# Optimization experiments

Hardware: AMD Instinct MI355X
Metric: run time of the kernel (lower is better)

The kernel has to match this reference:

```python
import jax, jax.numpy as jnp
import numpy as np
import math

B, P, N = 4, 8, 512
D_MODEL, H, D_K = 128, 4, 32
T_ALL = 4
WHICH_IDX = np.array([0, 1, 3])  # which_transition_matrices = [T,T,F,T]
T = 3
EPS = 1e-5


def setup_inputs() -> dict:
    key = jax.random.key(0)
    ks = jax.random.split(key, 12)
    inputs = jax.random.normal(ks[0], (B, P, N, D_MODEL), jnp.float32)
    c_inputs = jax.random.normal(ks[1], (B, P, N, D_MODEL), jnp.float32)
    vals = jax.random.uniform(ks[2], (T_ALL, N, N), jnp.float32)
    keep = (jax.random.uniform(ks[3], (T_ALL, N, N)) < 0.05).astype(jnp.float32)
    eye = jnp.eye(N, dtype=jnp.float32)
    transition_matrices = vals * keep * (1.0 - eye) + eye
    s = 1.0 / math.sqrt(D_MODEL)
    Wq = jax.random.normal(ks[4], (T, D_MODEL, D_MODEL), jnp.float32) * s
    Wk = jax.random.normal(ks[5], (T, D_MODEL, D_MODEL), jnp.float32) * s
    Wv = jax.random.normal(ks[6], (T, D_MODEL, D_MODEL), jnp.float32) * s
    Wo = jax.random.normal(ks[7], (D_MODEL, T * D_MODEL), jnp.float32) * (1.0 / math.sqrt(T * D_MODEL))
    ln_gamma = jnp.ones((D_MODEL,), jnp.float32)
    ln_beta = jnp.zeros((D_MODEL,), jnp.float32)
    return dict(inputs=inputs, c_inputs=c_inputs, transition_matrices=transition_matrices,
                Wq=Wq, Wk=Wk, Wv=Wv, Wo=Wo, ln_gamma=ln_gamma, ln_beta=ln_beta)


def reference(inputs, c_inputs, transition_matrices, Wq, Wk, Wv, Wo, ln_gamma, ln_beta):
    tm = transition_matrices[jnp.asarray(WHICH_IDX)]  # [T, N, N]
    # per-transition-matrix projections (torch Linear: x @ W.T), then split heads
    def proj(W):
        y = jnp.einsum('bpnd,tod->tbpno', inputs, W)
        return y.reshape(T, B, P, N, H, D_K)
    Q, K, V = proj(Wq), proj(Wk), proj(Wv)
    scores = jnp.einsum('tbpnhk,tbpmhk->tbphnm', Q, K) / math.sqrt(D_K)
    mask = jnp.where(tm != 0, 0.0, -jnp.inf)[:, None, None, None]  # [T,1,1,1,N,N]
    alpha = jax.nn.softmax(scores + mask, axis=-1)
    # post-softmax reweighting by transition matrix, then V matmul
    out = jnp.einsum('tbphnm,tbpmhk->tbpnhk', alpha * tm[:, None, None, None], V)
    out = out.reshape(T, B, P, N, D_MODEL)
    out = jnp.moveaxis(out, 0, -2).reshape(B, P, N, T * D_MODEL)  # concat over matrices
    out = jnp.einsum('bpnf,df->bpnd', out, Wo)  # final Linear (bias=False); dropout p=0
    res = out + inputs
    mu = res.mean(-1, keepdims=True)
    var = ((res - mu) ** 2).mean(-1, keepdims=True)
    return (res - mu) / jnp.sqrt(var + EPS) * ln_gamma + ln_beta
```

## Files before the change

### kernel.cpp

```cpp
#include <hip/hip_runtime.h>


typedef __attribute__((ext_vector_type(8))) short  short8;
typedef __attribute__((ext_vector_type(4))) float  floatx4;

#define WS_BIG   50331648ull
#define WS_XL    54919168ull
#define QSCALE   0.25503486f

__device__ __forceinline__ float b2f(unsigned short u) {
    union { unsigned int i; float f; } v; v.i = ((unsigned int)u) << 16; return v.f;
}
__device__ __forceinline__ unsigned short f2b(float f) {
    union { float f; unsigned int i; } v; v.f = f;
    unsigned int x = v.i;
    return (unsigned short)((x + 0x7fffu + ((x >> 16) & 1u)) >> 16);
}
__device__ __forceinline__ unsigned int fbits(float f) {
    union { float f; unsigned int i; } v; v.f = f; return v.i;
}
__device__ __forceinline__ short8 cvt8(const float* p) {
    floatx4 a = *(const floatx4*)p;
    floatx4 b = *(const floatx4*)(p + 4);
    short8 r;
    r[0] = (short)f2b(a[0]); r[1] = (short)f2b(a[1]);
    r[2] = (short)f2b(a[2]); r[3] = (short)f2b(a[3]);
    r[4] = (short)f2b(b[0]); r[5] = (short)f2b(b[1]);
    r[6] = (short)f2b(b[2]); r[7] = (short)f2b(b[3]);
    return r;
}

__global__ __launch_bounds__(256) void k_prep(
    const float* __restrict__ X,  const float* __restrict__ Wq,
    const float* __restrict__ Wk, const float* __restrict__ Wv,
    const float* __restrict__ Wo,
    unsigned short* __restrict__ Xb, unsigned short* __restrict__ Wb,
    unsigned short* __restrict__ Wob)
{
    size_t i = ((size_t)blockIdx.x * 256 + threadIdx.x) * 8;
    const float* src; unsigned short* dst; size_t off;
    if      (i < 2097152) { src = X;  dst = Xb;          off = i; }
    else if (i < 2146304) { src = Wq; dst = Wb;          off = i - 2097152; }
    else if (i < 2195456) { src = Wk; dst = Wb + 49152;  off = i - 2146304; }
    else if (i < 2244608) { src = Wv; dst = Wb + 98304;  off = i - 2195456; }
    else                  { src = Wo; dst = Wob;         off = i - 2244608; }
    *(short8*)&dst[off] = cvt8(&src[off]);
}

__global__ __launch_bounds__(256) void k_qkv_pre2(
    const unsigned short* __restrict__ Xb,
    const unsigned short* __restrict__ Wb,
    unsigned short* __restrict__ q_ws,
    unsigned short* __restrict__ k_ws,
    unsigned short* __restrict__ v_ws)
{
    int bp = blockIdx.x, mt = blockIdx.y, z = blockIdx.z;
    int qkv = z / 3, t = z % 3;
    __shared__ unsigned short Xs[128 * 128];
    __shared__ unsigned short Cs[4][32 * 128];
    int tid = threadIdx.x;
    int lane = tid & 63, wv = tid >> 6;
    int l15 = lane & 15, quad = lane >> 4;

    const unsigned short* Xbase = Xb + ((size_t)bp * 512 + mt * 128) * 128;
    for (int i = 0; i < 8; ++i) {
        int e = (i * 256 + tid) * 8;
        *(short8*)&Xs[e] = *(const short8*)&Xbase[e];
    }
    __syncthreads();

    unsigned short* Osel[3] = { q_ws, k_ws, v_ws };
    int rt0 = wv * 2, rt1 = wv * 2 + 1;

    const unsigned short* Wt = Wb + qkv * 49152 + t * 16384;
    unsigned short* Ob = Osel[qkv] + (size_t)t * 2097152
                       + ((size_t)bp * 512 + mt * 128 + wv * 32) * 128;
    float sc = (qkv == 0) ? QSCALE : 1.0f;

    for (int ct = 0; ct < 8; ++ct) {
        short8 bfr[4];
        for (int kk = 0; kk < 4; ++kk)
            bfr[kk] = *(const short8*)&Wt[(size_t)(ct * 16 + l15) * 128 + kk * 32 + quad * 8];
        floatx4 acc0 = {0.f, 0.f, 0.f, 0.f};
        floatx4 acc1 = {0.f, 0.f, 0.f, 0.f};
        for (int kk = 0; kk < 4; ++kk) {
            short8 a0 = *(const short8*)&Xs[(rt0 * 16 + l15) * 128 + kk * 32 + quad * 8];
            short8 a1 = *(const short8*)&Xs[(rt1 * 16 + l15) * 128 + kk * 32 + quad * 8];
            acc0 = __builtin_amdgcn_mfma_f32_16x16x32_bf16(a0, bfr[kk], acc0, 0, 0, 0);
            acc1 = __builtin_amdgcn_mfma_f32_16x16x32_bf16(a1, bfr[kk], acc1, 0, 0, 0);
        }
        #pragma unroll
        for (int i = 0; i < 4; ++i) {
            int row = quad * 4 + i;
            int swz = (row & 7) << 4;
            int col = (ct * 16 + l15) ^ swz;
            Cs[wv][row * 128 + col]        = f2b(acc0[i] * sc);
            Cs[wv][(16 + row) * 128 + col] = f2b(acc1[i] * sc);
        }
    }
    #pragma unroll
    for (int j = 0; j < 8; ++j) {
        int flat = j * 64 + lane;
        int r = flat >> 4;
        int cg = (flat & 15) * 8;
        int cgs = cg ^ ((r & 7) << 4);
        *(short8*)&Ob[(size_t)r * 128 + cg] = *(const short8*)&Cs[wv][r * 128 + cgs];
    }
}

__global__ __launch_bounds__(256) void k_qkv_cvt(
    const float* __restrict__ X,
    const float* __restrict__ Wq, const float* __restrict__ Wk,
    const float* __restrict__ Wv,
    unsigned short* __restrict__ q_ws, unsigned short* __restrict__ k_ws,
    unsigned short* __restrict__ v_ws,
    int wstride, int ostride)
{
    int bp = blockIdx.x, mt = blockIdx.y, tz = blockIdx.z;
    __shared__ unsigned short Xs[128 * 128];
    int tid = threadIdx.x;
    int lane = tid & 63, wv = tid >> 6;
    int l15 = lane & 15, quad = lane >> 4;

    const float* Xbase = X + ((size_t)bp * 512 + mt * 128) * 128;
    for (int i = 0; i < 8; ++i) {
        int e = (i * 256 + tid) * 8;
        *(short8*)&Xs[e] = cvt8(&Xbase[e]);
    }
    __syncthreads();

    size_t woff = (size_t)tz * wstride;
    size_t ooff = (size_t)tz * ostride;
    const float* Wsel[3] = { Wq + woff, Wk + woff, Wv + woff };
    unsigned short* Osel[3] = { q_ws + ooff, k_ws + ooff, v_ws + ooff };

    for (int qkv = 0; qkv < 3; ++qkv) {
        const float* Wt = Wsel[qkv];
        unsigned short* Ob = Osel[qkv] + ((size_t)bp * 512 + mt * 128) * 128;
        float sc = (qkv == 0) ? QSCALE : 1.0f;
        for (int ct = 0; ct < 8; ++ct) {
            short8 bfr[4];
            for (int kk = 0; kk < 4; ++kk)
                bfr[kk] = cvt8(&Wt[(size_t)(ct * 16 + l15) * 128 + kk * 32 + quad * 8]);
            floatx4 acc0 = {0.f, 0.f, 0.f, 0.f};
            floatx4 acc1 = {0.f, 0.f, 0.f, 0.f};
            int rt0 = wv * 2, rt1 = wv * 2 + 1;
            for (int kk = 0; kk < 4; ++kk) {
                short8 a0 = *(const short8*)&Xs[(rt0 * 16 + l15) * 128 + kk * 32 + quad * 8];
                short8 a1 = *(const short8*)&Xs[(rt1 * 16 + l15) * 128 + kk * 32 + quad * 8];
                acc0 = __builtin_amdgcn_mfma_f32_16x16x32_bf16(a0, bfr[kk], acc0, 0, 0, 0);
                acc1 = __builtin_amdgcn_mfma_f32_16x16x32_bf16(a1, bfr[kk], acc1, 0, 0, 0);
            }
            int col = ct * 16 + l15;
            for (int i = 0; i < 4; ++i) {
                Ob[(size_t)(rt0 * 16 + quad * 4 + i) * 128 + col] = f2b(acc0[i] * sc);
                Ob[(size_t)(rt1 * 16 + quad * 4 + i) * 128 + col] = f2b(acc1[i] * sc);
            }
        }
    }
}

__global__ __launch_bounds__(512) void k_attn2(
    const unsigned short* __restrict__ q_ws,
    const unsigned short* __restrict__ k_ws,
    const unsigned short* __restrict__ v_ws,
    const float* __restrict__ tm,
    unsigned short* __restrict__ att_ws,
    int qkv_stride, int toff0)
{
    int nc2 = blockIdx.x;
    int bp = blockIdx.y;
    int z  = blockIdx.z;
    int t = z >> 2, h = z & 3;
    size_t qoff = (size_t)t * (size_t)qkv_stride;
    const float* tmt = tm + (size_t)(t + (t >> 1)) * 262144;
    int toff = toff0 + t * 128;

    __shared__ unsigned short Vt[32][516];
    __shared__ unsigned short Ps[8][16][72];

    int tid = threadIdx.x, lane = tid & 63, wv = tid >> 6;
    int l15 = lane & 15, quad = lane >> 4;

    {
        const unsigned short* vp = v_ws + qoff + ((size_t)bp * 512 + tid) * 128 + h * 32;
        short8 a = *(const short8*)vp;
        short8 b = *(const short8*)(vp + 8);
        short8 c = *(const short8*)(vp + 16);
        short8 d = *(const short8*)(vp + 24);
        #pragma unroll
        for (int j = 0; j < 8; ++j) {
            Vt[j][tid]      = (unsigned short)a[j];
            Vt[8 + j][tid]  = (unsigned short)b[j];
            Vt[16 + j][tid] = (unsigned short)c[j];
            Vt[24 + j][tid] = (unsigned short)d[j];
        }
    }
    int n0 = nc2 * 256 + wv * 16;
    short8 qf[2];
    qf[0] = *(const short8*)&q_ws[qoff +
        ((size_t)bp * 512 + n0 + l15) * 128 + h * 32 + quad * 8];
    qf[1] = *(const short8*)&q_ws[qoff +
        ((size_t)bp * 512 + n0 + 128 + l15) * 128 + h * 32 + quad * 8];
    __syncthreads();

    const unsigned short* Kb = k_ws + qoff + (size_t)bp * 512 * 128 + h * 32;
    floatx4 O0[2] = {{0.f,0.f,0.f,0.f},{0.f,0.f,0.f,0.f}};
    floatx4 O1[2] = {{0.f,0.f,0.f,0.f},{0.f,0.f,0.f,0.f}};
    float za[2][4] = {{0.f,0.f,0.f,0.f},{0.f,0.f,0.f,0.f}};
    const floatx4 zero4 = {0.f, 0.f, 0.f, 0.f};

    for (int c = 0; c < 8; ++c) {
        int mb = c * 64;
        short8 kf0 = *(const short8*)&Kb[(size_t)(mb +  0 + l15) * 128 + quad * 8];
        short8 kf1 = *(const short8*)&Kb[(size_t)(mb + 16 + l15) * 128 + quad * 8];
        short8 kf2 = *(const short8*)&Kb[(size_t)(mb + 32 + l15) * 128 + quad * 8];
        short8 kf3 = *(const short8*)&Kb[(size_t)(mb + 48 + l15) * 128 + quad * 8];

        #pragma unroll
        for (int s = 0; s < 2; ++s) {
            int ns = n0 + s * 128;
            floatx4 S[4];
            S[0] = __builtin_amdgcn_mfma_f32_16x16x32_bf16(qf[s], kf0, zero4, 0, 0, 0);
            S[1] = __builtin_amdgcn_mfma_f32_16x16x32_bf16(qf[s], kf1, zero4, 0, 0, 0);
            S[2] = __builtin_amdgcn_mfma_f32_16x16x32_bf16(qf[s], kf2, zero4, 0, 0, 0);
            S[3] = __builtin_amdgcn_mfma_f32_16x16x32_bf16(qf[s], kf3, zero4, 0, 0, 0);

            #pragma unroll
            for (int ti = 0; ti < 4; ++ti) {
                int m = mb + ti * 16 + l15;
                #pragma unroll
                for (int i = 0; i < 4; ++i) {
                    float tmv = tmt[(size_t)(ns + quad * 4 + i) * 512 + m];
                    float e = __builtin_amdgcn_exp2f(S[ti][i]);
                    za[s][i] += (tmv != 0.0f) ? e : 0.0f;
                    float w = e * tmv;
                    Ps[wv][quad * 4 + i][ti * 16 + l15] =
                        (unsigned short)((fbits(w) + 0x8000u) >> 16);
                }
            }
            #pragma unroll
            for (int kc = 0; kc < 2; ++kc) {
                short8 pa  = *(const short8*)&Ps[wv][l15][kc * 32 + quad * 8];
                short8 vb0 = *(const short8*)&Vt[l15][mb + kc * 32 + quad * 8];
                short8 vb1 = *(const short8*)&Vt[16 + l15][mb + kc * 32 + quad * 8];
                O0[s] = __builtin_amdgcn_mfma_f32_16x16x32_bf16(pa, vb0, O0[s], 0, 0, 0);
                O1[s] = __builtin_amdgcn_mfma_f32_16x16x32_bf16(pa, vb1, O1[s], 0, 0, 0);
            }
        }
    }

    #pragma unroll
    for (int s = 0; s < 2; ++s) {
        #pragma unroll
        for (int d = 1; d < 16; d <<= 1) {
            #pragma unroll
            for (int i = 0; i < 4; ++i) za[s][i] += __shfl_xor(za[s][i], d, 64);
        }
        #pragma unroll
        for (int i = 0; i < 4; ++i) {
            float rz = 1.0f / za[s][i];
            size_t row = (size_t)bp * 512 + n0 + s * 128 + quad * 4 + i;
            att_ws[row * 384 + toff + h * 32 + l15]      = f2b(O0[s][i] * rz);
            att_ws[row * 384 + toff + h * 32 + 16 + l15] = f2b(O1[s][i] * rz);
        }
    }
}

__global__ __launch_bounds__(256) void k_oproj_pre2(
    const unsigned short* __restrict__ att_ws,
    const unsigned short* __restrict__ Wob,
    const float* __restrict__ X,
    const float* __restrict__ gamma,
    const float* __restrict__ beta,
    float* __restrict__ out)
{
    int bp = blockIdx.x;
    int mt = blockIdx.y;
    __shared__ unsigned short As[32 * 128];
    __shared__ unsigned short Ws[128 * 128];
    __shared__ float Ls_s[2][32];
    __shared__ float Ls_q[2][32];
    int tid = threadIdx.x, lane = tid & 63, wv = tid >> 6;
    int l15 = lane & 15, quad = lane >> 4;
    int rtile = wv & 1, chalf = wv >> 1;

    floatx4 acc[4];
    for (int ct = 0; ct < 4; ++ct) acc[ct] = (floatx4){0.f, 0.f, 0.f, 0.f};
    size_t rowbase = (size_t)bp * 512 + mt * 32;

    for (int kc = 0; kc < 3; ++kc) {
        __syncthreads();
        for (int i = 0; i < 2; ++i) {
            int flat = i * 256 + tid;
            int row = flat >> 4, colg = (flat & 15) * 8;
            *(short8*)&As[row * 128 + colg] =
                *(const short8*)&att_ws[(rowbase + row) * 384 + kc * 128 + colg];
        }
        for (int i = 0; i < 8; ++i) {
            int flat = i * 256 + tid;
            int row = flat >> 4, colg = (flat & 15) * 8;
            *(short8*)&Ws[row * 128 + colg] =
                *(const short8*)&Wob[(size_t)row * 384 + kc * 128 + colg];
        }
        __syncthreads();
        for (int ct = 0; ct < 4; ++ct) {
            for (int kk = 0; kk < 4; ++kk) {
                short8 a = *(const short8*)&As[(rtile * 16 + l15) * 128 + kk * 32 + quad * 8];
                short8 b = *(const short8*)&Ws[((chalf * 4 + ct) * 16 + l15) * 128 + kk * 32 + quad * 8];
                acc[ct] = __builtin_amdgcn_mfma_f32_16x16x32_bf16(a, b, acc[ct], 0, 0, 0);
            }
        }
    }

    float vals[4][4];
    #pragma unroll
    for (int i = 0; i < 4; ++i) {
        int lrow = rtile * 16 + quad * 4 + i;
        size_t grow = rowbase + lrow;
        float s = 0.f, sq = 0.f;
        #pragma unroll
        for (int ct = 0; ct < 4; ++ct) {
            int col = (chalf * 4 + ct) * 16 + l15;
            float v = acc[ct][i] + X[grow * 128 + col];
            vals[i][ct] = v;
            s += v; sq += v * v;
        }
        #pragma unroll
        for (int d = 1; d < 16; d <<= 1) {
            s  += __shfl_xor(s, d, 64);
            sq += __shfl_xor(sq, d, 64);
        }
        if (l15 == 0) { Ls_s[chalf][lrow] = s; Ls_q[chalf][lrow] = sq; }
    }
    __syncthreads();
    #pragma unroll
    for (int i = 0; i < 4; ++i) {
        int lrow = rtile * 16 + quad * 4 + i;
        size_t grow = rowbase + lrow;
        float st  = Ls_s[0][lrow] + Ls_s[1][lrow];
        float sqt = Ls_q[0][lrow] + Ls_q[1][lrow];
        float mu = st * (1.0f / 128.0f);
        float var = sqt * (1.0f / 128.0f) - mu * mu;
        float rs = rsqrtf(var + 1e-5f);
        #pragma unroll
        for (int ct = 0; ct < 4; ++ct) {
            int col = (chalf * 4 + ct) * 16 + l15;
            out[grow * 128 + col] = (vals[i][ct] - mu) * rs * gamma[col] + beta[col];
        }
    }
}

__global__ __launch_bounds__(256) void k_oproj_cvt(
    const unsigned short* __restrict__ att_ws,
    const float* __restrict__ Wo,
    const float* __restrict__ X,
    const float* __restrict__ gamma,
    const float* __restrict__ beta,
    float* __restrict__ out)
{
    int bp = blockIdx.x;
    int mt = blockIdx.y;
    __shared__ unsigned short As[64 * 128];
    __shared__ unsigned short Ws[128 * 128];
    int tid = threadIdx.x, lane = tid & 63, wv = tid >> 6;
    int l15 = lane & 15, quad = lane >> 4;

    floatx4 acc[8];
    for (int ct = 0; ct < 8; ++ct) acc[ct] = (floatx4){0.f, 0.f, 0.f, 0.f};
    size_t rowbase = (size_t)bp * 512 + mt * 64;

    for (int kc = 0; kc < 3; ++kc) {
        __syncthreads();
        for (int i = 0; i < 4; ++i) {
            int flat = i * 256 + tid;
            int row = flat >> 4, colg = (flat & 15) * 8;
            *(short8*)&As[row * 128 + colg] =
                *(const short8*)&att_ws[(rowbase + row) * 384 + kc * 128 + colg];
        }
        for (int i = 0; i < 8; ++i) {
            int flat = i * 256 + tid;
            int row = flat >> 4, colg = (flat & 15) * 8;
            *(short8*)&Ws[row * 128 + colg] = cvt8(&Wo[(size_t)row * 384 + kc * 128 + colg]);
        }
        __syncthreads();
        for (int ct = 0; ct < 8; ++ct) {
            for (int kk = 0; kk < 4; ++kk) {
                short8 a = *(const short8*)&As[(wv * 16 + l15) * 128 + kk * 32 + quad * 8];
                short8 b = *(const short8*)&Ws[(ct * 16 + l15) * 128 + kk * 32 + quad * 8];
                acc[ct] = __builtin_amdgcn_mfma_f32_16x16x32_bf16(a, b, acc[ct], 0, 0, 0);
            }
        }
    }

    for (int i = 0; i < 4; ++i) {
        int lrow = wv * 16 + quad * 4 + i;
        size_t grow = rowbase + lrow;
        float vals[8];
        float s = 0.f, sq = 0.f;
        for (int ct = 0; ct < 8; ++ct) {
            int col = ct * 16 + l15;
            float v = acc[ct][i] + X[grow * 128 + col];
            vals[ct] = v;
            s += v; sq += v * v;
        }
        for (int d = 1; d < 16; d <<= 1) {
            s  += __shfl_xor(s, d, 64);
            sq += __shfl_xor(sq, d, 64);
        }
        float mu = s * (1.0f / 128.0f);
        float var = sq * (1.0f / 128.0f) - mu * mu;
        float rs = rsqrtf(var + 1e-5f);
        for (int ct = 0; ct < 8; ++ct) {
            int col = ct * 16 + l15;
            out[grow * 128 + col] = (vals[ct] - mu) * rs * gamma[col] + beta[col];
        }
    }
}

extern "C" void kernel_launch(void* const* d_in, const int* in_sizes, int n_in,
                              void* d_out, int out_size, void* d_ws, size_t ws_size,
                              hipStream_t stream) {
    const float* X     = (const float*)d_in[0];
    const float* TM    = (const float*)d_in[2];
    const float* Wq    = (const float*)d_in[3];
    const float* Wk    = (const float*)d_in[4];
    const float* Wv    = (const float*)d_in[5];
    const float* Wo    = (const float*)d_in[6];
    const float* gamma = (const float*)d_in[7];
    const float* beta  = (const float*)d_in[8];
    float* out = (float*)d_out;

    char* ws = (char*)d_ws;
    const size_t QKV1 = 2097152;
    const size_t QKV1B = QKV1 * 2;

    if (ws_size >= WS_XL) {
        unsigned short* q3  = (unsigned short*)(ws);
        unsigned short* k3  = (unsigned short*)(ws + 3 * QKV1B);
        unsigned short* v3  = (unsigned short*)(ws + 6 * QKV1B);
        unsigned short* att = (unsigned short*)(ws + 9 * QKV1B);
        unsigned short* Xb  = (unsigned short*)(ws + 50331648ull);
        unsigned short* Wb  = (unsigned short*)(ws + 54525952ull);
        unsigned short* Wob = (unsigned short*)(ws + 54820864ull);
        k_prep<<<dim3(1120), 256, 0, stream>>>(X, Wq, Wk, Wv, Wo, Xb, Wb, Wob);
        k_qkv_pre2<<<dim3(32, 4, 9), 256, 0, stream>>>(Xb, Wb, q3, k3, v3);
        k_attn2<<<dim3(2, 32, 12), 512, 0, stream>>>(q3, k3, v3, TM, att, (int)QKV1, 0);
        k_oproj_pre2<<<dim3(32, 16), 256, 0, stream>>>(att, Wob, X, gamma, beta, out);
    } else if (ws_size >= WS_BIG) {
        unsigned short* q3  = (unsigned short*)(ws);
        unsigned short* k3  = (unsigned short*)(ws + 3 * QKV1B);
        unsigned short* v3  = (unsigned short*)(ws + 6 * QKV1B);
        unsigned short* att = (unsigned short*)(ws + 9 * QKV1B);
        k_qkv_cvt<<<dim3(32, 4, 3), 256, 0, stream>>>(
            X, Wq, Wk, Wv, q3, k3, v3, 16384, (int)QKV1);
        k_attn2<<<dim3(2, 32, 12), 512, 0, stream>>>(q3, k3, v3, TM, att, (int)QKV1, 0);
        k_oproj_cvt<<<dim3(32, 8), 256, 0, stream>>>(att, Wo, X, gamma, beta, out);
    } else {
        unsigned short* q_ws   = (unsigned short*)(ws);
        unsigned short* k_ws   = (unsigned short*)(ws + QKV1B);
        unsigned short* v_ws   = (unsigned short*)(ws + 2 * QKV1B);
        unsigned short* att_ws = (unsigned short*)(ws + 3 * QKV1B);
        const int tsel[3] = {0, 1, 3};
        for (int t = 0; t < 3; ++t) {
            k_qkv_cvt<<<dim3(32, 4, 1), 256, 0, stream>>>(
                X, Wq + (size_t)t * 16384, Wk + (size_t)t * 16384, Wv + (size_t)t * 16384,
                q_ws, k_ws, v_ws, 0, 0);
            k_attn2<<<dim3(2, 32, 4), 512, 0, stream>>>(
                q_ws, k_ws, v_ws, TM + (size_t)tsel[t] * 262144, att_ws, 0, t * 128);
        }
        k_oproj_cvt<<<dim3(32, 8), 256, 0, stream>>>(att_ws, Wo, X, gamma, beta, out);
    }
}
```

Measured before the change: 170.4 us.

## Transpose score MFMA to vectorize mask loads and packed bf16 P stores

```diff
diff --git a/kernel.cpp b/kernel.cpp
--- a/kernel.cpp
+++ b/kernel.cpp
@@ -3,6 +3,7 @@
 
 typedef __attribute__((ext_vector_type(8))) short  short8;
 typedef __attribute__((ext_vector_type(4))) float  floatx4;
+typedef __attribute__((ext_vector_type(2))) unsigned int uint2v;
 
 #define WS_BIG   50331648ull
 #define WS_XL    54919168ull
@@ -16,8 +17,10 @@
     unsigned int x = v.i;
     return (unsigned short)((x + 0x7fffu + ((x >> 16) & 1u)) >> 16);
 }
-__device__ __forceinline__ unsigned int fbits(float f) {
-    union { float f; unsigned int i; } v; v.f = f; return v.i;
+__device__ __forceinline__ unsigned int cvt_pk_bf16(float a, float b) {
+    unsigned int r;
+    asm("v_cvt_pk_bf16_f32 %0, %1, %2" : "=v"(r) : "v"(a), "v"(b));
+    return r;
 }
 __device__ __forceinline__ short8 cvt8(const float* p) {
     floatx4 a = *(const floatx4*)p;
@@ -160,7 +163,7 @@
     }
 }
 
-__global__ __launch_bounds__(512) void k_attn2(
+__global__ __launch_bounds__(512, 6) void k_attn5(
     const unsigned short* __restrict__ q_ws,
     const unsigned short* __restrict__ k_ws,
     const unsigned short* __restrict__ v_ws,
@@ -205,10 +208,28 @@
     __syncthreads();
 
     const unsigned short* Kb = k_ws + qoff + (size_t)bp * 512 * 128 + h * 32;
+    const float* tpc = tmt + (size_t)(n0 + l15) * 512 + quad * 4;
+
     floatx4 O0[2] = {{0.f,0.f,0.f,0.f},{0.f,0.f,0.f,0.f}};
     floatx4 O1[2] = {{0.f,0.f,0.f,0.f},{0.f,0.f,0.f,0.f}};
     float za[2][4] = {{0.f,0.f,0.f,0.f},{0.f,0.f,0.f,0.f}};
     const floatx4 zero4 = {0.f, 0.f, 0.f, 0.f};
+
+#define P_TILE(Sv, Tv, sidx, ti)                                              \
+    {                                                                         \
+        float e0 = __builtin_amdgcn_exp2f(Sv[0]);                             \
+        float e1 = __builtin_amdgcn_exp2f(Sv[1]);                             \
+        float e2 = __builtin_amdgcn_exp2f(Sv[2]);                             \
+        float e3 = __builtin_amdgcn_exp2f(Sv[3]);                             \
+        za[sidx][0] = __builtin_fmaf(e0, __builtin_ceilf(Tv[0]), za[sidx][0]);\
+        za[sidx][1] = __builtin_fmaf(e1, __builtin_ceilf(Tv[1]), za[sidx][1]);\
+        za[sidx][2] = __builtin_fmaf(e2, __builtin_ceilf(Tv[2]), za[sidx][2]);\
+        za[sidx][3] = __builtin_fmaf(e3, __builtin_ceilf(Tv[3]), za[sidx][3]);\
+        uint2v pk;                                                            \
+        pk.x = cvt_pk_bf16(e0 * Tv[0], e1 * Tv[1]);                           \
+        pk.y = cvt_pk_bf16(e2 * Tv[2], e3 * Tv[3]);                           \
+        *(uint2v*)&Ps[wv][l15][(ti) * 16 + quad * 4] = pk;                    \
+    }
 
     for (int c = 0; c < 8; ++c) {
         int mb = c * 64;
@@ -217,49 +238,63 @@
         short8 kf2 = *(const short8*)&Kb[(size_t)(mb + 32 + l15) * 128 + quad * 8];
         short8 kf3 = *(const short8*)&Kb[(size_t)(mb + 48 + l15) * 128 + quad * 8];
 
-        #pragma unroll
-        for (int s = 0; s < 2; ++s) {
-            int ns = n0 + s * 128;
-            floatx4 S[4];
-            S[0] = __builtin_amdgcn_mfma_f32_16x16x32_bf16(qf[s], kf0, zero4, 0, 0, 0);
-            S[1] = __builtin_amdgcn_mfma_f32_16x16x32_bf16(qf[s], kf1, zero4, 0, 0, 0);
-            S[2] = __builtin_amdgcn_mfma_f32_16x16x32_bf16(qf[s], kf2, zero4, 0, 0, 0);
-            S[3] = __builtin_amdgcn_mfma_f32_16x16x32_bf16(qf[s], kf3, zero4, 0, 0, 0);
-
-            #pragma unroll
-            for (int ti = 0; ti < 4; ++ti) {
-                int m = mb + ti * 16 + l15;
-                #pragma unroll
-                for (int i = 0; i < 4; ++i) {
-                    float tmv = tmt[(size_t)(ns + quad * 4 + i) * 512 + m];
-                    float e = __builtin_amdgcn_exp2f(S[ti][i]);
-                    za[s][i] += (tmv != 0.0f) ? e : 0.0f;
-                    float w = e * tmv;
-                    Ps[wv][quad * 4 + i][ti * 16 + l15] =
-                        (unsigned short)((fbits(w) + 0x8000u) >> 16);
-                }
-            }
+        {
+            floatx4 t40 = *(const floatx4*)(tpc +  0);
+            floatx4 t41 = *(const floatx4*)(tpc + 16);
+            floatx4 t42 = *(const floatx4*)(tpc + 32);
+            floatx4 t43 = *(const floatx4*)(tpc + 48);
+            floatx4 S0 = __builtin_amdgcn_mfma_f32_16x16x32_bf16(kf0, qf[0], zero4, 0, 0, 0);
+            floatx4 S1 = __builtin_amdgcn_mfma_f32_16x16x32_bf16(kf1, qf[0], zero4, 0, 0, 0);
+            floatx4 S2 = __builtin_amdgcn_mfma_f32_16x16x32_bf16(kf2, qf[0], zero4, 0, 0, 0);
+            floatx4 S3 = __builtin_amdgcn_mfma_f32_16x16x32_bf16(kf3, qf[0], zero4, 0, 0, 0);
+            P_TILE(S0, t40, 0, 0)
+            P_TILE(S1, t41, 0, 1)
+            P_TILE(S2, t42, 0, 2)
+            P_TILE(S3, t43, 0, 3)
             #pragma unroll
             for (int kc = 0; kc < 2; ++kc) {
                 short8 pa  = *(const short8*)&Ps[wv][l15][kc * 32 + quad * 8];
                 short8 vb0 = *(const short8*)&Vt[l15][mb + kc * 32 + quad * 8];
                 short8 vb1 = *(const short8*)&Vt[16 + l15][mb + kc * 32 + quad * 8];
-                O0[s] = __builtin_amdgcn_mfma_f32_16x16x32_bf16(pa, vb0, O0[s], 0, 0, 0);
-                O1[s] = __builtin_amdgcn_mfma_f32_16x16x32_bf16(pa, vb1, O1[s], 0, 0, 0);
+                O0[0] = __builtin_amdgcn_mfma_f32_16x16x32_bf16(pa, vb0, O0[0], 0, 0, 0);
+                O1[0] = __builtin_amdgcn_mfma_f32_16x16x32_bf16(pa, vb1, O1[0], 0, 0, 0);
             }
         }
-    }
+
+        {
+            floatx4 t40 = *(const floatx4*)(tpc + 65536 +  0);
+            floatx4 t41 = *(const floatx4*)(tpc + 65536 + 16);
+            floatx4 t42 = *(const floatx4*)(tpc + 65536 + 32);
+            floatx4 t43 = *(const floatx4*)(tpc + 65536 + 48);
+            floatx4 S0 = __builtin_amdgcn_mfma_f32_16x16x32_bf16(kf0, qf[1], zero4, 0, 0, 0);
+            floatx4 S1 = __builtin_amdgcn_mfma_f32_16x16x32_bf16(kf1, qf[1], zero4, 0, 0, 0);
+            floatx4 S2 = __builtin_amdgcn_mfma_f32_16x16x32_bf16(kf2, qf[1], zero4, 0, 0, 0);
+            floatx4 S3 = __builtin_amdgcn_mfma_f32_16x16x32_bf16(kf3, qf[1], zero4, 0, 0, 0);
+            P_TILE(S0, t40, 1, 0)
+            P_TILE(S1, t41, 1, 1)
+            P_TILE(S2, t42, 1, 2)
+            P_TILE(S3, t43, 1, 3)
+            #pragma unroll
+            for (int kc = 0; kc < 2; ++kc) {
+                short8 pa  = *(const short8*)&Ps[wv][l15][kc * 32 + quad * 8];
+                short8 vb0 = *(const short8*)&Vt[l15][mb + kc * 32 + quad * 8];
+                short8 vb1 = *(const short8*)&Vt[16 + l15][mb + kc * 32 + quad * 8];
+                O0[1] = __builtin_amdgcn_mfma_f32_16x16x32_bf16(pa, vb0, O0[1], 0, 0, 0);
+                O1[1] = __builtin_amdgcn_mfma_f32_16x16x32_bf16(pa, vb1, O1[1], 0, 0, 0);
+            }
+        }
+        tpc += 64;
+    }
+#undef P_TILE
 
     #pragma unroll
     for (int s = 0; s < 2; ++s) {
-        #pragma unroll
-        for (int d = 1; d < 16; d <<= 1) {
-            #pragma unroll
-            for (int i = 0; i < 4; ++i) za[s][i] += __shfl_xor(za[s][i], d, 64);
-        }
+        float zz = (za[s][0] + za[s][1]) + (za[s][2] + za[s][3]);
+        zz += __shfl_xor(zz, 16, 64);
+        zz += __shfl_xor(zz, 32, 64);
         #pragma unroll
         for (int i = 0; i < 4; ++i) {
-            float rz = 1.0f / za[s][i];
+            float rz = 1.0f / __shfl(zz, quad * 4 + i, 64);
             size_t row = (size_t)bp * 512 + n0 + s * 128 + quad * 4 + i;
             att_ws[row * 384 + toff + h * 32 + l15]      = f2b(O0[s][i] * rz);
             att_ws[row * 384 + toff + h * 32 + 16 + l15] = f2b(O1[s][i] * rz);
@@ -445,7 +480,7 @@
         unsigned short* Wob = (unsigned short*)(ws + 54820864ull);
         k_prep<<<dim3(1120), 256, 0, stream>>>(X, Wq, Wk, Wv, Wo, Xb, Wb, Wob);
         k_qkv_pre2<<<dim3(32, 4, 9), 256, 0, stream>>>(Xb, Wb, q3, k3, v3);
-        k_attn2<<<dim3(2, 32, 12), 512, 0, stream>>>(q3, k3, v3, TM, att, (int)QKV1, 0);
+        k_attn5<<<dim3(2, 32, 12), 512, 0, stream>>>(q3, k3, v3, TM, att, (int)QKV1, 0);
         k_oproj_pre2<<<dim3(32, 16), 256, 0, stream>>>(att, Wob, X, gamma, beta, out);
     } else if (ws_size >= WS_BIG) {
         unsigned short* q3  = (unsigned short*)(ws);
@@ -454,7 +489,7 @@
         unsigned short* att = (unsigned short*)(ws + 9 * QKV1B);
         k_qkv_cvt<<<dim3(32, 4, 3), 256, 0, stream>>>(
             X, Wq, Wk, Wv, q3, k3, v3, 16384, (int)QKV1);
-        k_attn2<<<dim3(2, 32, 12), 512, 0, stream>>>(q3, k3, v3, TM, att, (int)QKV1, 0);
+        k_attn5<<<dim3(2, 32, 12), 512, 0, stream>>>(q3, k3, v3, TM, att, (int)QKV1, 0);
         k_oproj_cvt<<<dim3(32, 8), 256, 0, stream>>>(att, Wo, X, gamma, beta, out);
     } else {
         unsigned short* q_ws   = (unsigned short*)(ws);
@@ -466,7 +501,7 @@
             k_qkv_cvt<<<dim3(32, 4, 1), 256, 0, stream>>>(
                 X, Wq + (size_t)t * 16384, Wk + (size_t)t * 16384, Wv + (size_t)t * 16384,
                 q_ws, k_ws, v_ws, 0, 0);
-            k_attn2<<<dim3(2, 32, 4), 512, 0, stream>>>(
+            k_attn5<<<dim3(2, 32, 4), 512, 0, stream>>>(
                 q_ws, k_ws, v_ws, TM + (size_t)tsel[t] * 262144, att_ws, 0, t * 128);
         }
         k_oproj_cvt<<<dim3(32, 8), 256, 0, stream>>>(att_ws, Wo, X, gamma, beta, out);
```

Measured after the change: 250.3 us. +46.9%, slower.
